# Kernel tuning notes

Hardware: AMD Instinct MI355X
Metric: run time of the kernel (lower is better)

The kernel has to match this reference:

```python
import jax, jax.numpy as jnp
import numpy as np

FEATS = 768
HEAD = 12


def _phi(t):
    # elu feature map + 1 (guarantees positivity)
    return jax.nn.elu(t) + 1.0


def setup_inputs() -> dict:
    key = jax.random.key(0)
    ks = jax.random.split(key, 9)
    f = FEATS
    s = 1.0 / np.sqrt(f)
    x = jax.random.normal(ks[0], (4, 4096, f), dtype=jnp.float32)
    # weights stored as [in, out] so projection is x @ W + b
    Wq = jax.random.normal(ks[1], (f, f), dtype=jnp.float32) * s
    bq = jax.random.normal(ks[2], (f,), dtype=jnp.float32) * 0.01
    Wk = jax.random.normal(ks[3], (f, f), dtype=jnp.float32) * s
    bk = jax.random.normal(ks[4], (f,), dtype=jnp.float32) * 0.01
    Wv = jax.random.normal(ks[5], (f, f), dtype=jnp.float32) * s
    bv = jax.random.normal(ks[6], (f,), dtype=jnp.float32) * 0.01
    Wo = jax.random.normal(ks[7], (f, f), dtype=jnp.float32) * s
    bo = jax.random.normal(ks[8], (f,), dtype=jnp.float32) * 0.01
    return {"x": x, "Wq": Wq, "bq": bq, "Wk": Wk, "bk": bk,
            "Wv": Wv, "bv": bv, "Wo": Wo, "bo": bo}


def reference(x, Wq, bq, Wk, bk, Wv, bv, Wo, bo):
    b, n, f = x.shape
    h = HEAD
    d = f // h
    # project and split heads: [b, h, n, d]
    def heads(t):
        return t.reshape(b, n, h, d).transpose(0, 2, 1, 3)
    q = _phi(heads(x @ Wq + bq))
    k = _phi(heads(x @ Wk + bk))
    v = heads(x @ Wv + bv)
    # kv summary: [b, h, d, d] (sum over sequence)
    kv = jnp.einsum('bhnd,bhne->bhde', k, v)
    # normalizer: z[b,h,l] = 1 / (q[b,h,l,:] . sum_n k[b,h,n,:])  (no eps, as in source)
    ksum = k.sum(axis=2)                      # [b, h, d]
    z = 1.0 / jnp.einsum('bhld,bhd->bhl', q, ksum)  # [b, h, n]
    num = jnp.einsum('bhld,bhde->bhle', q, kv)      # [b, h, n, d]
    normed = num * z[..., None]                     # [b, h, n, d]
    out = normed.transpose(0, 2, 1, 3).reshape(b, n, f)  # [b, n, f]
    return out @ Wo + bo  # dropout p=0.0 -> identity
```

## Files before the change

kernel.cpp:

```cpp
#include <hip/hip_runtime.h>
#include <cstdint>
#include <cstddef>

#define DEVI __device__ __forceinline__

typedef short    shortx8 __attribute__((ext_vector_type(8)));
typedef short    shortx4 __attribute__((ext_vector_type(4)));
typedef __bf16   bf16x8  __attribute__((ext_vector_type(8)));
typedef float    floatx4 __attribute__((ext_vector_type(4)));

DEVI unsigned short f2b(float f) {
    union { float f; unsigned u; } a; a.f = f;
    unsigned r = a.u + 0x7fffu + ((a.u >> 16) & 1u);
    return (unsigned short)(r >> 16);
}
DEVI float b2f(unsigned short u) {
    union { unsigned u; float f; } a; a.u = ((unsigned)u) << 16;
    return a.f;
}

DEVI floatx4 mfma_bf16(bf16x8 a, bf16x8 b, floatx4 c) {
    return __builtin_amdgcn_mfma_f32_16x16x32_bf16(a, b, c, 0, 0, 0);
}

DEVI void glds16(const ushort* g, ushort* l) {
    __builtin_amdgcn_global_load_lds(
        (const __attribute__((address_space(1))) void*)g,
        (__attribute__((address_space(3))) void*)l, 16, 0, 0);
}

__global__ void k_cvt(const float* __restrict__ x, ushort* __restrict__ xb) {
    size_t i = ((size_t)blockIdx.x * 256 + threadIdx.x) * 8;
    float4 v0 = *(const float4*)(x + i);
    float4 v1 = *(const float4*)(x + i + 4);
    shortx8 o;
    o[0] = (short)f2b(v0.x); o[1] = (short)f2b(v0.y);
    o[2] = (short)f2b(v0.z); o[3] = (short)f2b(v0.w);
    o[4] = (short)f2b(v1.x); o[5] = (short)f2b(v1.y);
    o[6] = (short)f2b(v1.z); o[7] = (short)f2b(v1.w);
    *(shortx8*)(xb + i) = o;
}

__global__ void k_packw(const float* __restrict__ Wq, const float* __restrict__ Wk,
                        const float* __restrict__ Wv, const float* __restrict__ Wo,
                        ushort* __restrict__ Wt, ushort* __restrict__ Wot) {
    const int zi = blockIdx.z;
    const float* W = (zi == 0) ? Wq : (zi == 1) ? Wk : (zi == 2) ? Wv : Wo;
    __shared__ float tile[64][65];
    const int i0 = blockIdx.x * 64, j0 = blockIdx.y * 64;
    const int t = threadIdx.x;
    const int c = t & 63, r4 = t >> 6;
    for (int rr = r4; rr < 64; rr += 4)
        tile[rr][c] = W[(size_t)(i0 + rr) * 768 + j0 + c];
    __syncthreads();
    ushort* dst = (zi < 3) ? (Wt + (size_t)(zi * 768) * 768) : Wot;
    for (int jj = r4; jj < 64; jj += 4)
        dst[(size_t)(j0 + jj) * 768 + i0 + c] = f2b(tile[c][jj]);
}

__global__ void k_bias(const float* __restrict__ bq, const float* __restrict__ bk,
                       const float* __restrict__ bv, float* __restrict__ bqkv) {
    int j = blockIdx.x * 256 + threadIdx.x;
    if (j >= 2304) return;
    const float* src = (j < 768) ? bq : (j < 1536) ? bk : bv;
    bqkv[j] = src[j % 768];
}

template <int MODE>
__global__ __launch_bounds__(256, 2) void k_gemm(
    const ushort* __restrict__ A, const ushort* __restrict__ Bt,
    const float* __restrict__ bias, void* __restrict__ Cout, int Ncols) {
    constexpr int K = 768;
    __shared__ ushort As[128 * 32];
    __shared__ ushort Bs[128 * 32];
    const int m0 = blockIdx.x * 128;
    const int n0 = blockIdx.y * 128;
    const int tid = threadIdx.x;
    const int w = tid >> 6, lane = tid & 63;

    const int srow = lane >> 2;
    const int scol = ((lane & 3) ^ ((srow >> 1) & 3)) * 8;
    const ushort* ag0 = A  + (size_t)(m0 + w * 32 +      srow) * K + scol;
    const ushort* ag1 = A  + (size_t)(m0 + w * 32 + 16 + srow) * K + scol;
    const ushort* bg0 = Bt + (size_t)(n0 + w * 32 +      srow) * K + scol;
    const ushort* bg1 = Bt + (size_t)(n0 + w * 32 + 16 + srow) * K + scol;
    ushort* al0 = As + (w * 32     ) * 32;
    ushort* al1 = As + (w * 32 + 16) * 32;
    ushort* bl0 = Bs + (w * 32     ) * 32;
    ushort* bl1 = Bs + (w * 32 + 16) * 32;

    const int rBase = (w >> 1) * 64;
    const int nBase = (w & 1) * 64;
    const int fr = lane & 15;
    const int fks = (((lane >> 4) ^ ((fr >> 1) & 3))) * 8;

    floatx4 acc[4][4] = {};

    for (int k0 = 0; k0 < K; k0 += 32) {
        glds16(ag0 + k0, al0);
        glds16(ag1 + k0, al1);
        glds16(bg0 + k0, bl0);
        glds16(bg1 + k0, bl1);
        __syncthreads();
        bf16x8 af[4], bf[4];
#pragma unroll
        for (int rt = 0; rt < 4; ++rt)
            af[rt] = *(const bf16x8*)(As + (rBase + rt * 16 + fr) * 32 + fks);
#pragma unroll
        for (int nt = 0; nt < 4; ++nt)
            bf[nt] = *(const bf16x8*)(Bs + (nBase + nt * 16 + fr) * 32 + fks);
#pragma unroll
        for (int rt = 0; rt < 4; ++rt)
#pragma unroll
            for (int nt = 0; nt < 4; ++nt)
                acc[rt][nt] = mfma_bf16(af[rt], bf[nt], acc[rt][nt]);
        __syncthreads();
    }

#pragma unroll
    for (int rt = 0; rt < 4; ++rt) {
#pragma unroll
        for (int nt = 0; nt < 4; ++nt) {
#pragma unroll
            for (int r = 0; r < 4; ++r) {
                int m = m0 + rBase + rt * 16 + (lane >> 4) * 4 + r;
                int n = n0 + nBase + nt * 16 + fr;
                float v = acc[rt][nt][r] + bias[n];
                if (MODE == 0) {
                    if (n < 1536) v = (v > 0.f) ? (v + 1.f) : __expf(v);
                    ((ushort*)Cout)[(size_t)m * Ncols + n] = f2b(v);
                } else {
                    ((float*)Cout)[(size_t)m * Ncols + n] = v;
                }
            }
        }
    }
}

__global__ __launch_bounds__(256) void k_kv(const ushort* __restrict__ QKV,
                                            float* __restrict__ kvp) {
    const int bh = blockIdx.x, s = blockIdx.y;
    const int bb = bh / 12, head = bh % 12;
    __shared__ ushort kS[64 * 68];
    __shared__ ushort vS[64 * 68];
    const int t = threadIdx.x, w = t >> 6, lane = t & 63;
    const int fr = lane & 15, fk = (lane >> 4) * 8;

    floatx4 acc[5] = {};
    const int n_ld = t >> 2, c16 = (t & 3) * 16;
    const ushort* base = QKV + (size_t)(bb * 4096 + s * 512) * 2304 + 768 + head * 64 + c16;

    for (int rr = 0; rr < 8; ++rr) {
        if (rr) __syncthreads();
        {
            const ushort* kp = base + (size_t)(rr * 64 + n_ld) * 2304;
            union { shortx8 v8; shortx4 v4[2]; } k0, k1, v0, v1;
            k0.v8 = *(const shortx8*)(kp);
            k1.v8 = *(const shortx8*)(kp + 8);
            v0.v8 = *(const shortx8*)(kp + 768);
            v1.v8 = *(const shortx8*)(kp + 776);
            ushort* kd = kS + n_ld * 68 + c16;
            ushort* vd = vS + n_ld * 68 + c16;
            *(shortx4*)(kd)     = k0.v4[0]; *(shortx4*)(kd + 4)  = k0.v4[1];
            *(shortx4*)(kd + 8) = k1.v4[0]; *(shortx4*)(kd + 12) = k1.v4[1];
            *(shortx4*)(vd)     = v0.v4[0]; *(shortx4*)(vd + 4)  = v0.v4[1];
            *(shortx4*)(vd + 8) = v1.v4[0]; *(shortx4*)(vd + 12) = v1.v4[1];
        }
        __syncthreads();
#pragma unroll
        for (int kl = 0; kl < 64; kl += 32) {
            union { bf16x8 v; ushort u[8]; } bfr, afr[4];
#pragma unroll
            for (int i = 0; i < 8; ++i) {
                int n = kl + fk + i;
                bfr.u[i] = kS[n * 68 + w * 16 + fr];
#pragma unroll
                for (int mt = 0; mt < 4; ++mt)
                    afr[mt].u[i] = vS[n * 68 + mt * 16 + fr];
            }
            union { bf16x8 v; ushort u[8]; } ones;
            ushort ov = (fr == 0) ? (ushort)0x3F80 : (ushort)0;
#pragma unroll
            for (int i = 0; i < 8; ++i) ones.u[i] = ov;
#pragma unroll
            for (int mt = 0; mt < 4; ++mt)
                acc[mt] = mfma_bf16(afr[mt].v, bfr.v, acc[mt]);
            acc[4] = mfma_bf16(ones.v, bfr.v, acc[4]);
        }
    }

    float* dst = kvp + ((size_t)bh * 8 + s) * (65 * 64);
#pragma unroll
    for (int mt = 0; mt < 4; ++mt)
#pragma unroll
        for (int r = 0; r < 4; ++r)
            dst[(mt * 16 + (lane >> 4) * 4 + r) * 64 + w * 16 + fr] = acc[mt][r];
    if (lane < 16) dst[64 * 64 + w * 16 + lane] = acc[4][0];
}

__global__ void k_kvred(const float* __restrict__ kvp, ushort* __restrict__ kvb) {
    int t4 = (blockIdx.x * 256 + threadIdx.x) * 4;
    int bh = t4 / 4160, rem = t4 % 4160;
    const float* p = kvp + (size_t)bh * 8 * 4160 + rem;
    float4 sum = {0.f, 0.f, 0.f, 0.f};
    for (int i = 0; i < 8; ++i) {
        float4 a = *(const float4*)(p + (size_t)i * 4160);
        sum.x += a.x; sum.y += a.y; sum.z += a.z; sum.w += a.w;
    }
    shortx4 o;
    o[0] = (short)f2b(sum.x); o[1] = (short)f2b(sum.y);
    o[2] = (short)f2b(sum.z); o[3] = (short)f2b(sum.w);
    *(shortx4*)(kvb + t4) = o;
}

__global__ __launch_bounds__(256) void k_num(const ushort* __restrict__ QKV,
                                             const ushort* __restrict__ kvb,
                                             ushort* __restrict__ normed) {
    const int bh = blockIdx.x, l0 = blockIdx.y * 128;
    const int bb = bh / 12, head = bh % 12;
    __shared__ ushort qsh[128 * 72];
    __shared__ ushort kvT[80 * 72];
    __shared__ float dnm[128];
    const int t = threadIdx.x, w = t >> 6, lane = t & 63;

    {
        const ushort* kvbb = kvb + (size_t)bh * 4160;
        int c8 = (t & 7) * 8;
        for (int r0 = (t >> 3); r0 < 65; r0 += 32)
            *(shortx8*)(kvT + r0 * 72 + c8) = *(const shortx8*)(kvbb + r0 * 64 + c8);
    }
    for (int idx = t; idx < 15 * 72; idx += 256) kvT[65 * 72 + idx] = 0;

    const ushort* qg = QKV + (size_t)(bb * 4096 + l0) * 2304 + head * 64;
    {
        int row = t >> 3, c8 = (t & 7) * 8;
#pragma unroll
        for (int i = 0; i < 4; ++i) {
            shortx8 v = *(const shortx8*)(qg + (size_t)(i * 32 + row) * 2304 + c8);
            *(shortx8*)(qsh + (i * 32 + row) * 72 + c8) = v;
        }
    }
    __syncthreads();

    const int fr = lane & 15, fk = (lane >> 4) * 8;
    floatx4 acc[2][5] = {};
#pragma unroll
    for (int kc = 0; kc < 2; ++kc) {
        bf16x8 a[2], b[5];
#pragma unroll
        for (int rt = 0; rt < 2; ++rt)
            a[rt] = *(const bf16x8*)(qsh + (w * 32 + rt * 16 + fr) * 72 + kc * 32 + fk);
#pragma unroll
        for (int nt = 0; nt < 5; ++nt)
            b[nt] = *(const bf16x8*)(kvT + (nt * 16 + fr) * 72 + kc * 32 + fk);
#pragma unroll
        for (int rt = 0; rt < 2; ++rt)
#pragma unroll
            for (int nt = 0; nt < 5; ++nt)
                acc[rt][nt] = mfma_bf16(a[rt], b[nt], acc[rt][nt]);
    }
    if (fr == 0) {
#pragma unroll
        for (int rt = 0; rt < 2; ++rt)
#pragma unroll
            for (int r = 0; r < 4; ++r)
                dnm[w * 32 + rt * 16 + (lane >> 4) * 4 + r] = acc[rt][4][r];
    }
    __syncthreads();
#pragma unroll
    for (int rt = 0; rt < 2; ++rt) {
#pragma unroll
        for (int r = 0; r < 4; ++r) {
            int ml = w * 32 + rt * 16 + (lane >> 4) * 4 + r;
            float z = 1.f / dnm[ml];
            size_t base = (size_t)(bb * 4096 + l0 + ml) * 768 + head * 64;
#pragma unroll
            for (int nt = 0; nt < 4; ++nt)
                normed[base + nt * 16 + fr] = f2b(acc[rt][nt][r] * z);
        }
    }
}

extern "C" void kernel_launch(void* const* d_in, const int* in_sizes, int n_in,
                              void* d_out, int out_size, void* d_ws, size_t ws_size,
                              hipStream_t stream) {
    const float* x  = (const float*)d_in[0];
    const float* Wq = (const float*)d_in[1];
    const float* bq = (const float*)d_in[2];
    const float* Wk = (const float*)d_in[3];
    const float* bk = (const float*)d_in[4];
    const float* Wv = (const float*)d_in[5];
    const float* bv = (const float*)d_in[6];
    const float* Wo = (const float*)d_in[7];
    const float* bo = (const float*)d_in[8];

    char* ws = (char*)d_ws;
    ushort* Xb   = (ushort*)(ws);
    ushort* Wt   = (ushort*)(ws + 25165824);
    ushort* Wot  = (ushort*)(ws + 28704768);
    float*  bqkv = (float*)(ws + 29884416);
    ushort* QKV  = (ushort*)(ws + 29893632);
    float*  kvp  = (float*)(ws + 105391104);
    ushort* kvb  = (ushort*)(ws + 111780864);
    ushort* normed = Xb;

    k_cvt  <<<dim3(6144),        256, 0, stream>>>(x, Xb);
    k_packw<<<dim3(12, 12, 4),   256, 0, stream>>>(Wq, Wk, Wv, Wo, Wt, Wot);
    k_bias <<<dim3(9),           256, 0, stream>>>(bq, bk, bv, bqkv);
    k_gemm<0><<<dim3(128, 18),   256, 0, stream>>>(Xb, Wt, bqkv, (void*)QKV, 2304);
    k_kv   <<<dim3(48, 8),       256, 0, stream>>>(QKV, kvp);
    k_kvred<<<dim3(195),         256, 0, stream>>>(kvp, kvb);
    k_num  <<<dim3(48, 32),      256, 0, stream>>>(QKV, kvb, normed);
    k_gemm<1><<<dim3(128, 6),    256, 0, stream>>>(normed, Wot, bo, d_out, 768);
}
```

Before: 250.6 us.

## Merge prep kernels, deepen GEMM K-tile to 64, repad kv LDS stride

```diff
diff --git a/kernel.cpp b/kernel.cpp
--- a/kernel.cpp
+++ b/kernel.cpp
@@ -6,6 +6,7 @@
 
 typedef short    shortx8 __attribute__((ext_vector_type(8)));
 typedef short    shortx4 __attribute__((ext_vector_type(4)));
+typedef short    shortx2 __attribute__((ext_vector_type(2)));
 typedef __bf16   bf16x8  __attribute__((ext_vector_type(8)));
 typedef float    floatx4 __attribute__((ext_vector_type(4)));
 
@@ -29,41 +30,43 @@
         (__attribute__((address_space(3))) void*)l, 16, 0, 0);
 }
 
-__global__ void k_cvt(const float* __restrict__ x, ushort* __restrict__ xb) {
-    size_t i = ((size_t)blockIdx.x * 256 + threadIdx.x) * 8;
-    float4 v0 = *(const float4*)(x + i);
-    float4 v1 = *(const float4*)(x + i + 4);
-    shortx8 o;
-    o[0] = (short)f2b(v0.x); o[1] = (short)f2b(v0.y);
-    o[2] = (short)f2b(v0.z); o[3] = (short)f2b(v0.w);
-    o[4] = (short)f2b(v1.x); o[5] = (short)f2b(v1.y);
-    o[6] = (short)f2b(v1.z); o[7] = (short)f2b(v1.w);
-    *(shortx8*)(xb + i) = o;
-}
-
-__global__ void k_packw(const float* __restrict__ Wq, const float* __restrict__ Wk,
-                        const float* __restrict__ Wv, const float* __restrict__ Wo,
-                        ushort* __restrict__ Wt, ushort* __restrict__ Wot) {
-    const int zi = blockIdx.z;
-    const float* W = (zi == 0) ? Wq : (zi == 1) ? Wk : (zi == 2) ? Wv : Wo;
+__global__ void k_prep(const float* __restrict__ x, ushort* __restrict__ xb,
+                       const float* __restrict__ Wq, const float* __restrict__ Wk,
+                       const float* __restrict__ Wv, const float* __restrict__ Wo,
+                       ushort* __restrict__ Wt, ushort* __restrict__ Wot,
+                       const float* __restrict__ bq, const float* __restrict__ bk,
+                       const float* __restrict__ bv, float* __restrict__ bqkv) {
     __shared__ float tile[64][65];
-    const int i0 = blockIdx.x * 64, j0 = blockIdx.y * 64;
-    const int t = threadIdx.x;
-    const int c = t & 63, r4 = t >> 6;
-    for (int rr = r4; rr < 64; rr += 4)
-        tile[rr][c] = W[(size_t)(i0 + rr) * 768 + j0 + c];
-    __syncthreads();
-    ushort* dst = (zi < 3) ? (Wt + (size_t)(zi * 768) * 768) : Wot;
-    for (int jj = r4; jj < 64; jj += 4)
-        dst[(size_t)(j0 + jj) * 768 + i0 + c] = f2b(tile[c][jj]);
-}
-
-__global__ void k_bias(const float* __restrict__ bq, const float* __restrict__ bk,
-                       const float* __restrict__ bv, float* __restrict__ bqkv) {
-    int j = blockIdx.x * 256 + threadIdx.x;
-    if (j >= 2304) return;
-    const float* src = (j < 768) ? bq : (j < 1536) ? bk : bv;
-    bqkv[j] = src[j % 768];
+    const int bid = blockIdx.x, t = threadIdx.x;
+    if (bid < 6144) {
+        size_t i = ((size_t)bid * 256 + t) * 8;
+        float4 v0 = *(const float4*)(x + i);
+        float4 v1 = *(const float4*)(x + i + 4);
+        shortx8 o;
+        o[0] = (short)f2b(v0.x); o[1] = (short)f2b(v0.y);
+        o[2] = (short)f2b(v0.z); o[3] = (short)f2b(v0.w);
+        o[4] = (short)f2b(v1.x); o[5] = (short)f2b(v1.y);
+        o[6] = (short)f2b(v1.z); o[7] = (short)f2b(v1.w);
+        *(shortx8*)(xb + i) = o;
+    } else if (bid < 6720) {
+        int pid = bid - 6144;
+        int zi = pid / 144, rem = pid % 144;
+        const float* W = (zi == 0) ? Wq : (zi == 1) ? Wk : (zi == 2) ? Wv : Wo;
+        const int i0 = (rem / 12) * 64, j0 = (rem % 12) * 64;
+        const int c = t & 63, r4 = t >> 6;
+        for (int rr = r4; rr < 64; rr += 4)
+            tile[rr][c] = W[(size_t)(i0 + rr) * 768 + j0 + c];
+        __syncthreads();
+        ushort* dst = (zi < 3) ? (Wt + (size_t)(zi * 768) * 768) : Wot;
+        for (int jj = r4; jj < 64; jj += 4)
+            dst[(size_t)(j0 + jj) * 768 + i0 + c] = f2b(tile[c][jj]);
+    } else {
+        int j = (bid - 6720) * 256 + t;
+        if (j < 2304) {
+            const float* src = (j < 768) ? bq : (j < 1536) ? bk : bv;
+            bqkv[j] = src[j % 768];
+        }
+    }
 }
 
 template <int MODE>
@@ -71,49 +74,53 @@
     const ushort* __restrict__ A, const ushort* __restrict__ Bt,
     const float* __restrict__ bias, void* __restrict__ Cout, int Ncols) {
     constexpr int K = 768;
-    __shared__ ushort As[128 * 32];
-    __shared__ ushort Bs[128 * 32];
+    __shared__ ushort As[128 * 64];
+    __shared__ ushort Bs[128 * 64];
     const int m0 = blockIdx.x * 128;
     const int n0 = blockIdx.y * 128;
     const int tid = threadIdx.x;
     const int w = tid >> 6, lane = tid & 63;
 
-    const int srow = lane >> 2;
-    const int scol = ((lane & 3) ^ ((srow >> 1) & 3)) * 8;
-    const ushort* ag0 = A  + (size_t)(m0 + w * 32 +      srow) * K + scol;
-    const ushort* ag1 = A  + (size_t)(m0 + w * 32 + 16 + srow) * K + scol;
-    const ushort* bg0 = Bt + (size_t)(n0 + w * 32 +      srow) * K + scol;
-    const ushort* bg1 = Bt + (size_t)(n0 + w * 32 + 16 + srow) * K + scol;
-    ushort* al0 = As + (w * 32     ) * 32;
-    ushort* al1 = As + (w * 32 + 16) * 32;
-    ushort* bl0 = Bs + (w * 32     ) * 32;
-    ushort* bl1 = Bs + (w * 32 + 16) * 32;
+    const int lr = lane >> 3;
+    const int lc = ((lane & 7) ^ lr) * 8;
+    const ushort* ag[4]; const ushort* bg[4]; ushort* al[4]; ushort* bl[4];
+#pragma unroll
+    for (int i = 0; i < 4; ++i) {
+        ag[i] = A  + (size_t)(m0 + w * 32 + i * 8 + lr) * K + lc;
+        bg[i] = Bt + (size_t)(n0 + w * 32 + i * 8 + lr) * K + lc;
+        al[i] = As + (w * 32 + i * 8) * 64;
+        bl[i] = Bs + (w * 32 + i * 8) * 64;
+    }
 
     const int rBase = (w >> 1) * 64;
     const int nBase = (w & 1) * 64;
     const int fr = lane & 15;
-    const int fks = (((lane >> 4) ^ ((fr >> 1) & 3))) * 8;
+    const int q4 = lane >> 4;
 
     floatx4 acc[4][4] = {};
 
-    for (int k0 = 0; k0 < K; k0 += 32) {
-        glds16(ag0 + k0, al0);
-        glds16(ag1 + k0, al1);
-        glds16(bg0 + k0, bl0);
-        glds16(bg1 + k0, bl1);
+    for (int k0 = 0; k0 < K; k0 += 64) {
+#pragma unroll
+        for (int i = 0; i < 4; ++i) glds16(ag[i] + k0, al[i]);
+#pragma unroll
+        for (int i = 0; i < 4; ++i) glds16(bg[i] + k0, bl[i]);
         __syncthreads();
-        bf16x8 af[4], bf[4];
-#pragma unroll
-        for (int rt = 0; rt < 4; ++rt)
-            af[rt] = *(const bf16x8*)(As + (rBase + rt * 16 + fr) * 32 + fks);
-#pragma unroll
-        for (int nt = 0; nt < 4; ++nt)
-            bf[nt] = *(const bf16x8*)(Bs + (nBase + nt * 16 + fr) * 32 + fks);
-#pragma unroll
-        for (int rt = 0; rt < 4; ++rt)
+#pragma unroll
+        for (int kc = 0; kc < 2; ++kc) {
+            const int off = ((kc * 4 + q4) ^ (fr & 7)) * 8;
+            bf16x8 af[4], bf[4];
+#pragma unroll
+            for (int rt = 0; rt < 4; ++rt)
+                af[rt] = *(const bf16x8*)(As + (rBase + rt * 16 + fr) * 64 + off);
 #pragma unroll
             for (int nt = 0; nt < 4; ++nt)
-                acc[rt][nt] = mfma_bf16(af[rt], bf[nt], acc[rt][nt]);
+                bf[nt] = *(const bf16x8*)(Bs + (nBase + nt * 16 + fr) * 64 + off);
+#pragma unroll
+            for (int rt = 0; rt < 4; ++rt)
+#pragma unroll
+                for (int nt = 0; nt < 4; ++nt)
+                    acc[rt][nt] = mfma_bf16(af[rt], bf[nt], acc[rt][nt]);
+        }
         __syncthreads();
     }
 
@@ -123,7 +130,7 @@
         for (int nt = 0; nt < 4; ++nt) {
 #pragma unroll
             for (int r = 0; r < 4; ++r) {
-                int m = m0 + rBase + rt * 16 + (lane >> 4) * 4 + r;
+                int m = m0 + rBase + rt * 16 + q4 * 4 + r;
                 int n = n0 + nBase + nt * 16 + fr;
                 float v = acc[rt][nt][r] + bias[n];
                 if (MODE == 0) {
@@ -141,8 +148,8 @@
                                             float* __restrict__ kvp) {
     const int bh = blockIdx.x, s = blockIdx.y;
     const int bb = bh / 12, head = bh % 12;
-    __shared__ ushort kS[64 * 68];
-    __shared__ ushort vS[64 * 68];
+    __shared__ ushort kS[64 * 70];
+    __shared__ ushort vS[64 * 70];
     const int t = threadIdx.x, w = t >> 6, lane = t & 63;
     const int fr = lane & 15, fk = (lane >> 4) * 8;
 
@@ -154,17 +161,20 @@
         if (rr) __syncthreads();
         {
             const ushort* kp = base + (size_t)(rr * 64 + n_ld) * 2304;
-            union { shortx8 v8; shortx4 v4[2]; } k0, k1, v0, v1;
+            union { shortx8 v8; shortx2 v2[4]; } k0, k1, v0, v1;
             k0.v8 = *(const shortx8*)(kp);
             k1.v8 = *(const shortx8*)(kp + 8);
             v0.v8 = *(const shortx8*)(kp + 768);
             v1.v8 = *(const shortx8*)(kp + 776);
-            ushort* kd = kS + n_ld * 68 + c16;
-            ushort* vd = vS + n_ld * 68 + c16;
-            *(shortx4*)(kd)     = k0.v4[0]; *(shortx4*)(kd + 4)  = k0.v4[1];
-            *(shortx4*)(kd + 8) = k1.v4[0]; *(shortx4*)(kd + 12) = k1.v4[1];
-            *(shortx4*)(vd)     = v0.v4[0]; *(shortx4*)(vd + 4)  = v0.v4[1];
-            *(shortx4*)(vd + 8) = v1.v4[0]; *(shortx4*)(vd + 12) = v1.v4[1];
+            ushort* kd = kS + n_ld * 70 + c16;
+            ushort* vd = vS + n_ld * 70 + c16;
+#pragma unroll
+            for (int i = 0; i < 4; ++i) {
+                *(shortx2*)(kd + 2 * i)     = k0.v2[i];
+                *(shortx2*)(kd + 8 + 2 * i) = k1.v2[i];
+                *(shortx2*)(vd + 2 * i)     = v0.v2[i];
+                *(shortx2*)(vd + 8 + 2 * i) = v1.v2[i];
+            }
         }
         __syncthreads();
 #pragma unroll
@@ -173,10 +183,10 @@
 #pragma unroll
             for (int i = 0; i < 8; ++i) {
                 int n = kl + fk + i;
-                bfr.u[i] = kS[n * 68 + w * 16 + fr];
+                bfr.u[i] = kS[n * 70 + w * 16 + fr];
 #pragma unroll
                 for (int mt = 0; mt < 4; ++mt)
-                    afr[mt].u[i] = vS[n * 68 + mt * 16 + fr];
+                    afr[mt].u[i] = vS[n * 70 + mt * 16 + fr];
             }
             union { bf16x8 v; ushort u[8]; } ones;
             ushort ov = (fr == 0) ? (ushort)0x3F80 : (ushort)0;
@@ -304,12 +314,11 @@
     ushort* kvb  = (ushort*)(ws + 111780864);
     ushort* normed = Xb;
 
-    k_cvt  <<<dim3(6144),        256, 0, stream>>>(x, Xb);
-    k_packw<<<dim3(12, 12, 4),   256, 0, stream>>>(Wq, Wk, Wv, Wo, Wt, Wot);
-    k_bias <<<dim3(9),           256, 0, stream>>>(bq, bk, bv, bqkv);
-    k_gemm<0><<<dim3(128, 18),   256, 0, stream>>>(Xb, Wt, bqkv, (void*)QKV, 2304);
-    k_kv   <<<dim3(48, 8),       256, 0, stream>>>(QKV, kvp);
-    k_kvred<<<dim3(195),         256, 0, stream>>>(kvp, kvb);
-    k_num  <<<dim3(48, 32),      256, 0, stream>>>(QKV, kvb, normed);
-    k_gemm<1><<<dim3(128, 6),    256, 0, stream>>>(normed, Wot, bo, d_out, 768);
-}
+    k_prep <<<dim3(6729),      256, 0, stream>>>(x, Xb, Wq, Wk, Wv, Wo, Wt, Wot,
+                                                 bq, bk, bv, bqkv);
+    k_gemm<0><<<dim3(128, 18), 256, 0, stream>>>(Xb, Wt, bqkv, (void*)QKV, 2304);
+    k_kv   <<<dim3(48, 8),     256, 0, stream>>>(QKV, kvp);
+    k_kvred<<<dim3(195),       256, 0, stream>>>(kvp, kvb);
+    k_num  <<<dim3(48, 32),    256, 0, stream>>>(QKV, kvb, normed);
+    k_gemm<1><<<dim3(128, 6),  256, 0, stream>>>(normed, Wot, bo, d_out, 768);
+}
```

Result: faster. 237.8 us (-5.1%).
